# Kernel tuning notes

Measured on AMD Instinct MI355X. Metric: run time of the kernel, lower is better.

Reference implementation:

```python
import jax, jax.numpy as jnp
import numpy as np

N_NODES = 50000
N_EDGES = 800000
D_IN = 8
D_MODEL = 128
N_CLASSES = 2


def gcn_conv(x, W, b, src, dst, n_nodes):
    # PyG GCNConv: h = x @ W; add self-loops; D^{-1/2} A D^{-1/2} aggregation; + bias
    h = x @ W  # [N, D]
    deg = jax.ops.segment_sum(jnp.ones(src.shape[0], h.dtype), dst, num_segments=n_nodes) + 1.0  # +1 self-loop
    dinv = jax.lax.rsqrt(deg)  # deg >= 1 always
    norm = dinv[src] * dinv[dst]  # [E]
    agg = jax.ops.segment_sum(h[src] * norm[:, None], dst, num_segments=n_nodes)
    agg = agg + h * (dinv * dinv)[:, None]  # self-loop term, norm_ii = dinv_i^2
    return agg + b


def setup_inputs() -> dict:
    key = jax.random.key(0)
    ks = jax.random.split(key, 10)
    x = jax.random.normal(ks[0], (N_NODES, D_IN), jnp.float32)
    edge_index = jax.random.randint(ks[1], (2, N_EDGES), 0, N_NODES, jnp.int64 if jax.config.jax_enable_x64 else jnp.int32)
    def glorot(k, shape):
        lim = np.sqrt(6.0 / (shape[0] + shape[1]))
        return jax.random.uniform(k, shape, jnp.float32, -lim, lim)
    return {
        "x": x,
        "edge_index": edge_index,
        "W1": glorot(ks[2], (D_IN, D_MODEL)),
        "b1": jnp.zeros((D_MODEL,), jnp.float32),
        "W2": glorot(ks[3], (D_MODEL, D_MODEL)),
        "b2": jnp.zeros((D_MODEL,), jnp.float32),
        "Wlin1": glorot(ks[4], (2 * D_MODEL, D_MODEL)),
        "blin1": jnp.zeros((D_MODEL,), jnp.float32),
        "Wfin": glorot(ks[5], (D_MODEL, N_CLASSES)),
        "bfin": jnp.zeros((N_CLASSES,), jnp.float32),
    }


def reference(x, edge_index, W1, b1, W2, b2, Wlin1, blin1, Wfin, bfin):
    src, dst = edge_index[0], edge_index[1]
    n = x.shape[0]
    h = jax.nn.relu(gcn_conv(x, W1, b1, src, dst, n))
    h = jax.nn.relu(gcn_conv(h, W2, b2, src, dst, n))
    xpair = jnp.concatenate((h[src], h[dst]), axis=1)  # [E, 2*D]
    xpair = jax.nn.relu(xpair @ Wlin1 + blin1)
    logits = xpair @ Wfin + bfin  # [E, C]
    return jax.nn.log_softmax(logits, axis=1)
```

## Files before the change

kernel.cpp:

```cpp
#include <hip/hip_runtime.h>
#include <stdint.h>
#include <math.h>

#define D 128

typedef unsigned short u16;
typedef __attribute__((ext_vector_type(8))) short bf16x8;
typedef __attribute__((ext_vector_type(4))) float f32x4;
typedef __attribute__((ext_vector_type(2))) float f32x2;

union BU { uint4 u; bf16x8 s; };

__device__ __forceinline__ unsigned f2bf_pk(float a, float b) {
    union { float f; unsigned u; } x, y; x.f = a; y.f = b;
    unsigned ra = x.u + 0x7FFF + ((x.u >> 16) & 1);
    unsigned rb = y.u + 0x7FFF + ((y.u >> 16) & 1);
    return (ra >> 16) | (rb & 0xFFFF0000u);
}
__device__ __forceinline__ u16 f2bf(float f) {
    union { float f; unsigned u; } x; x.f = f;
    unsigned r = x.u + 0x7FFF + ((x.u >> 16) & 1);
    return (u16)(r >> 16);
}
__device__ __forceinline__ f32x2 bf2f2v(unsigned u) {
    union { unsigned w[2]; f32x2 v; } t;
    t.w[0] = u << 16; t.w[1] = u & 0xFFFF0000u;
    return t.v;
}
__device__ __forceinline__ f32x2 vmax0(f32x2 a) {
    return __builtin_elementwise_max(a, (f32x2)(0.f));
}
__device__ __forceinline__ int padded4(int deg) {
    return (deg + 3) & ~3;
}


__global__ __launch_bounds__(256) void k_degree8(const int* __restrict__ dst, int E,
                                                 int* __restrict__ hist8, u16* __restrict__ rank, int N,
                                                 int eb4,
                                                 const float* __restrict__ W2, const float* __restrict__ Wlin,
                                                 unsigned* __restrict__ wswz) {
    int b = blockIdx.x;
    int t = threadIdx.x;
    if (b < eb4) {
        int i = b * 256 + t;
        int copy = b & 7;
        int E4 = E >> 2;
        if (i < E4) {
            int4 d = ((const int4*)dst)[i];
            int* h = hist8 + copy * N;
            ushort4 rk;
            rk.x = (u16)atomicAdd(&h[d.x], 1);
            rk.y = (u16)atomicAdd(&h[d.y], 1);
            rk.z = (u16)atomicAdd(&h[d.z], 1);
            rk.w = (u16)atomicAdd(&h[d.w], 1);
            ((ushort4*)rank)[i] = rk;
        }
        if (i == 0) {
            for (int j = E4 * 4; j < E; ++j) rank[j] = (u16)atomicAdd(&hist8[dst[j]], 1);
        }
    } else {
        int tid = (b - eb4) * 256 + t;
        int m = tid >> 13;
        int r = tid & 8191;
        int jp = r & 3;
        int lane = (r >> 2) & 63;
        int ct = (r >> 8) & 7;
        int kc = r >> 11;
        int k0 = kc * 32 + (lane >> 4) * 8 + 2 * jp;
        int n = ct * 16 + (lane & 15);
        const float* srcp = (m == 0) ? W2 : (Wlin + (m - 1) * 16384);
        wswz[tid] = f2bf_pk(srcp[k0 * 128 + n], srcp[(k0 + 1) * 128 + n]);
    }
}

__global__ __launch_bounds__(256) void k_xcdoff_bsum(int* __restrict__ hist8, int* __restrict__ degi,
                                                     float* __restrict__ dinv, int* __restrict__ bsum, int N,
                                                     const float* __restrict__ x, float* __restrict__ xs) {
    __shared__ int ws[4];
    int t = threadIdx.x;
    int i = blockIdx.x * 256 + t;
    int pd = 0;
    if (i < N) {
        int run = 0;
#pragma unroll
        for (int j = 0; j < 8; ++j) {
            int c = hist8[j * N + i];
            hist8[j * N + i] = run;
            run += c;
        }
        degi[i] = run;
        float dv = rsqrtf((float)run + 1.0f);
        dinv[i] = dv;
        const float4* xp = (const float4*)(x + (size_t)i * 8);
        float4 a0 = xp[0], a1 = xp[1];
        float4 w0 = make_float4(dv * a0.x, dv * a0.y, dv * a0.z, dv * a0.w);
        float4 w1 = make_float4(dv * a1.x, dv * a1.y, dv * a1.z, dv * a1.w);
        float4* xo = (float4*)(xs + (size_t)i * 8);
        xo[0] = w0; xo[1] = w1;
        pd = padded4(run);
    } else if (i == N) {
        float4 z = make_float4(0.f, 0.f, 0.f, 0.f);
        float4* xo = (float4*)(xs + (size_t)N * 8);
        xo[0] = z; xo[1] = z;
    }
    int v = pd;
#pragma unroll
    for (int off = 1; off < 64; off <<= 1) v += __shfl_xor(v, off, 64);
    if ((t & 63) == 0) ws[t >> 6] = v;
    __syncthreads();
    if (t == 0) bsum[blockIdx.x] = ws[0] + ws[1] + ws[2] + ws[3];
}

__global__ __launch_bounds__(256) void k_scan_final(const int* __restrict__ degi, const int* __restrict__ bsum,
                                                    int* __restrict__ prow, int N, int* __restrict__ hist8,
                                                    int nb) {
    __shared__ int s[256];
    __shared__ int sb[256];
    int t = threadIdx.x;
    sb[t] = (t < nb) ? bsum[t] : 0;
    __syncthreads();
    for (int off = 1; off < 256; off <<= 1) {
        int v = (t >= off) ? sb[t - off] : 0;
        __syncthreads();
        sb[t] += v;
        __syncthreads();
    }
    int boff = (blockIdx.x == 0) ? 0 : sb[blockIdx.x - 1];

    int i = blockIdx.x * 256 + t;
    int pd = (i < N) ? padded4(degi[i]) : 0;
    s[t] = pd;
    __syncthreads();
    for (int off = 1; off < 256; off <<= 1) {
        int v = (t >= off) ? s[t - off] : 0;
        __syncthreads();
        s[t] += v;
        __syncthreads();
    }
    if (i < N) {
        int p = boff + ((t == 0) ? 0 : s[t - 1]);
        prow[i] = p;
#pragma unroll
        for (int j = 0; j < 8; ++j) hist8[j * N + i] += p;
    }
    if (blockIdx.x == (unsigned)(nb - 1) && t == 0) prow[N] = sb[nb - 1];
}


__global__ __launch_bounds__(256) void k_scatter_fill(
        const int* __restrict__ src, const int* __restrict__ dst, int E,
        const int* __restrict__ prow, const int* __restrict__ hist8, const u16* __restrict__ rank,
        const int* __restrict__ degi,
        u16* __restrict__ colsrc, int N, int eb4) {
    int t = threadIdx.x;
    int b = blockIdx.x;
    if (b < eb4) {
        int i = b * 256 + t;
        int E4 = E >> 2;
        if (i < E4) {
            int copy = b & 7;
            int4 d = ((const int4*)dst)[i];
            int4 s4 = ((const int4*)src)[i];
            ushort4 rk = ((const ushort4*)rank)[i];
            const int* h = hist8 + copy * N;
            colsrc[h[d.x] + rk.x] = (u16)s4.x;
            colsrc[h[d.y] + rk.y] = (u16)s4.y;
            colsrc[h[d.z] + rk.z] = (u16)s4.z;
            colsrc[h[d.w] + rk.w] = (u16)s4.w;
        }
        if (i == 0) {
            for (int j = E4 * 4; j < E; ++j)
                colsrc[hist8[dst[j]] + rank[j]] = (u16)src[j];
        }
    } else {
        int n = (b - eb4) * 256 + t;
        if (n < N) {
            int lo = prow[n];
            int deg = degi[n];
            int pd = padded4(deg);
            for (int j = deg; j < pd; ++j) colsrc[lo + j] = (u16)N;
        }
        if (b == eb4 && t == 0) {
            int P = prow[N];
            for (int j = 0; j < 16; ++j) colsrc[P + j] = (u16)N;
        }
    }
}

#define HROW 136


__global__ __launch_bounds__(256) void k_agg1gemm(
        const float* __restrict__ xs, const int* __restrict__ prow,
        const u16* __restrict__ colsrc, const float* __restrict__ dinv,
        const float* __restrict__ b1, const float* __restrict__ W1,
        const uint4* __restrict__ wB0, u16* __restrict__ out0, int N) {
    __shared__ float W1s[8 * 128];
    __shared__ float b1s[128];
    __shared__ float ys[16][8];
    __shared__ u16 hs[16 * HROW];
    int t = threadIdx.x;
    int wv = t >> 6;
    int lane = t & 63;
    int sub = lane >> 4;
    int r = lane & 15;
    int base = blockIdx.x * 16;

    for (int idx = t; idx < 8 * 128; idx += 256) W1s[idx] = W1[idx];
    if (t < 128) b1s[t] = b1[t];

    int i = base + wv * 4 + sub;
    if (i < N) {
        float acc[8];
#pragma unroll
        for (int f = 0; f < 8; ++f) acc[f] = 0.f;
        int lo = prow[i], hiP = prow[i + 1];
        for (int k = lo + r; k < hiP; k += 16) {
            int cj = colsrc[k];
            const float4* xr = (const float4*)(xs + (size_t)cj * 8);
            float4 u0 = xr[0], u1 = xr[1];
            acc[0] += u0.x; acc[1] += u0.y; acc[2] += u0.z; acc[3] += u0.w;
            acc[4] += u1.x; acc[5] += u1.y; acc[6] += u1.z; acc[7] += u1.w;
        }
#pragma unroll
        for (int off = 1; off < 16; off <<= 1) {
#pragma unroll
            for (int f = 0; f < 8; ++f) acc[f] += __shfl_xor(acc[f], off, 64);
        }
        const float4* xi = (const float4*)(xs + (size_t)i * 8);
        float4 s0 = xi[0], s1 = xi[1];
        float di = dinv[i];
        acc[0] = di * (acc[0] + s0.x); acc[1] = di * (acc[1] + s0.y);
        acc[2] = di * (acc[2] + s0.z); acc[3] = di * (acc[3] + s0.w);
        acc[4] = di * (acc[4] + s1.x); acc[5] = di * (acc[5] + s1.y);
        acc[6] = di * (acc[6] + s1.z); acc[7] = di * (acc[7] + s1.w);
        if (r < 8) ys[wv * 4 + sub][r] = acc[r];
    }
    __syncthreads();

    {
        int node16 = t >> 4;
        int cseg = (t & 15) * 8;
        if (base + node16 < N) {
            float yv[8];
#pragma unroll
            for (int f = 0; f < 8; ++f) yv[f] = ys[node16][f];
            float o[8];
#pragma unroll
            for (int c = 0; c < 8; ++c) {
                float s = b1s[cseg + c];
#pragma unroll
                for (int f = 0; f < 8; ++f) s += yv[f] * W1s[f * 128 + cseg + c];
                o[c] = fmaxf(s, 0.f);
            }
            uint4 ov;
            ov.x = f2bf_pk(o[0], o[1]);
            ov.y = f2bf_pk(o[2], o[3]);
            ov.z = f2bf_pk(o[4], o[5]);
            ov.w = f2bf_pk(o[6], o[7]);
            *(uint4*)(hs + node16 * HROW + cseg) = ov;
        } else {
            *(uint4*)(hs + node16 * HROW + cseg) = make_uint4(0, 0, 0, 0);
        }
    }
    __syncthreads();

    int quad = lane >> 4;
    int l15 = lane & 15;
    int ct0 = wv * 2;

    f32x4 accA[2];
#pragma unroll
    for (int q = 0; q < 2; ++q) accA[q] = (f32x4){0.f, 0.f, 0.f, 0.f};

    const uint4* hrow = (const uint4*)(hs + l15 * HROW);
#pragma unroll
    for (int kc = 0; kc < 4; ++kc) {
        BU a; a.u = hrow[kc * 4 + quad];
#pragma unroll
        for (int q = 0; q < 2; ++q) {
            BU b0; b0.u = wB0[(kc * 8 + ct0 + q) * 64 + lane];
            accA[q] = __builtin_amdgcn_mfma_f32_16x16x32_bf16(a.s, b0.s, accA[q], 0, 0, 0);
        }
    }
#pragma unroll
    for (int reg = 0; reg < 4; ++reg) {
        int node = base + quad * 4 + reg;
        if (node >= N) continue;
        float sc = dinv[node];
#pragma unroll
        for (int q = 0; q < 2; ++q) {
            int colj = (ct0 + q) * 16 + l15;
            out0[(size_t)node * 128 + colj] = f2bf(accA[q][reg] * sc);
        }
    }
    if (blockIdx.x == 0 && t < 64) ((unsigned*)out0)[(size_t)N * 64 + t] = 0;
}


template <bool DUAL>
__global__ __launch_bounds__(256) void k_aggemm(const uint4* __restrict__ g, const int* __restrict__ prow,
                                                const u16* __restrict__ colsrc, const float* __restrict__ dinv,
                                                const float* __restrict__ biasH,
                                                const uint4* __restrict__ wB0, const uint4* __restrict__ wB1,
                                                const float* __restrict__ bias1,
                                                u16* __restrict__ out0, u16* __restrict__ out1, int N) {
    __shared__ u16 hs[16 * HROW];
    int t = threadIdx.x;
    int wv = t >> 6;
    int lane = t & 63;
    int sub = lane >> 4;
    int r = lane & 15;
    int base = blockIdx.x * 16;

    for (int nd = 0; nd < 4; ++nd) {
        int i = base + wv * 4 + nd;
        int lrow = wv * 4 + nd;
        if (i < N) {
            f32x2 acc2[4];
#pragma unroll
            for (int j = 0; j < 4; ++j) acc2[j] = (f32x2)(0.f);
            int lo = prow[i], hiP = prow[i + 1];
            int idx = lo + sub;
            int c0 = colsrc[idx];
            int c1 = (idx + 4 < hiP) ? colsrc[idx + 4] : N;
            int c2 = (idx + 8 < hiP) ? colsrc[idx + 8] : N;
            uint4 v0 = g[c0 * 16 + r];
            uint4 v1 = g[c1 * 16 + r];
            for (int k = lo; k < hiP; k += 4) {
                int c3 = (idx + 12 < hiP) ? colsrc[idx + 12] : N;
                uint4 v2 = g[c2 * 16 + r];
                acc2[0] += bf2f2v(v0.x);
                acc2[1] += bf2f2v(v0.y);
                acc2[2] += bf2f2v(v0.z);
                acc2[3] += bf2f2v(v0.w);
                v0 = v1; v1 = v2; c2 = c3; idx += 4;
            }
#pragma unroll
            for (int j = 0; j < 4; ++j) {
                acc2[j].x += __shfl_xor(acc2[j].x, 16, 64);
                acc2[j].y += __shfl_xor(acc2[j].y, 16, 64);
                acc2[j].x += __shfl_xor(acc2[j].x, 32, 64);
                acc2[j].y += __shfl_xor(acc2[j].y, 32, 64);
            }
            if (sub == 0) {
                uint4 sv = g[i * 16 + r];
                acc2[0] += bf2f2v(sv.x);
                acc2[1] += bf2f2v(sv.y);
                acc2[2] += bf2f2v(sv.z);
                acc2[3] += bf2f2v(sv.w);
                float di = dinv[i];
                float4 b0 = ((const float4*)biasH)[r * 2];
                float4 b1v = ((const float4*)biasH)[r * 2 + 1];
                float r0 = fmaxf(acc2[0].x * di + b0.x, 0.f);
                float r1 = fmaxf(acc2[0].y * di + b0.y, 0.f);
                float r2 = fmaxf(acc2[1].x * di + b0.z, 0.f);
                float r3 = fmaxf(acc2[1].y * di + b0.w, 0.f);
                float r4 = fmaxf(acc2[2].x * di + b1v.x, 0.f);
                float r5 = fmaxf(acc2[2].y * di + b1v.y, 0.f);
                float r6 = fmaxf(acc2[3].x * di + b1v.z, 0.f);
                float r7 = fmaxf(acc2[3].y * di + b1v.w, 0.f);
                uint4 o;
                o.x = f2bf_pk(r0, r1);
                o.y = f2bf_pk(r2, r3);
                o.z = f2bf_pk(r4, r5);
                o.w = f2bf_pk(r6, r7);
                *(uint4*)(hs + lrow * HROW + r * 8) = o;
            }
        } else if (sub == 0) {
            *(uint4*)(hs + lrow * HROW + r * 8) = make_uint4(0, 0, 0, 0);
        }
    }
    __syncthreads();

    int quad = lane >> 4;
    int l15 = lane & 15;
    int ct0 = wv * 2;

    f32x4 accA[2], accB[2];
#pragma unroll
    for (int q = 0; q < 2; ++q) { accA[q] = (f32x4){0.f, 0.f, 0.f, 0.f}; accB[q] = (f32x4){0.f, 0.f, 0.f, 0.f}; }

    const uint4* hrow = (const uint4*)(hs + l15 * HROW);
#pragma unroll
    for (int kc = 0; kc < 4; ++kc) {
        BU a; a.u = hrow[kc * 4 + quad];
#pragma unroll
        for (int q = 0; q < 2; ++q) {
            BU b0; b0.u = wB0[(kc * 8 + ct0 + q) * 64 + lane];
            accA[q] = __builtin_amdgcn_mfma_f32_16x16x32_bf16(a.s, b0.s, accA[q], 0, 0, 0);
            if (DUAL) {
                BU b1; b1.u = wB1[(kc * 8 + ct0 + q) * 64 + lane];
                accB[q] = __builtin_amdgcn_mfma_f32_16x16x32_bf16(a.s, b1.s, accB[q], 0, 0, 0);
            }
        }
    }
#pragma unroll
    for (int reg = 0; reg < 4; ++reg) {
        int node = base + quad * 4 + reg;
        if (node >= N) continue;
        float sc = DUAL ? 1.0f : dinv[node];
#pragma unroll
        for (int q = 0; q < 2; ++q) {
            int colj = (ct0 + q) * 16 + l15;
            out0[(size_t)node * 128 + colj] = f2bf(accA[q][reg] * sc);
            if (DUAL) out1[(size_t)node * 128 + colj] = f2bf(accB[q][reg] + bias1[colj]);
        }
    }
    if (blockIdx.x == 0 && t < 64) ((unsigned*)out0)[(size_t)N * 64 + t] = 0;
}


__global__ __launch_bounds__(256) void k_edge(const uint4* __restrict__ a, const uint4* __restrict__ c,
                                              const int* __restrict__ src, const int* __restrict__ dst,
                                              const float* __restrict__ Wfin, const float* __restrict__ bfin,
                                              float* __restrict__ out, int E) {
    int t = threadIdx.x;
    int g = t >> 4;
    int r = t & 15;
    int base = blockIdx.x * 64 + g * 4;

    f32x2 wd[4];
    const float4* wvp = (const float4*)Wfin;
#pragma unroll
    for (int q = 0; q < 4; ++q) {
        float4 m = wvp[r * 4 + q];
        wd[q] = (f32x2){m.x - m.y, m.z - m.w};
    }
    float bd = bfin[0] - bfin[1];

    int4 s4, d4;
    if (base + 3 < E) {
        s4 = ((const int4*)src)[blockIdx.x * 16 + g];
        d4 = ((const int4*)dst)[blockIdx.x * 16 + g];
    } else {
        int e0 = base, e1 = base + 1, e2 = base + 2, e3 = base + 3;
        s4.x = (e0 < E) ? src[e0] : 0; d4.x = (e0 < E) ? dst[e0] : 0;
        s4.y = (e1 < E) ? src[e1] : 0; d4.y = (e1 < E) ? dst[e1] : 0;
        s4.z = (e2 < E) ? src[e2] : 0; d4.z = (e2 < E) ? dst[e2] : 0;
        s4.w = (e3 < E) ? src[e3] : 0; d4.w = (e3 < E) ? dst[e3] : 0;
    }

    uint4 av[4], cv[4];
    av[0] = a[(size_t)s4.x * 16 + r];  cv[0] = c[(size_t)d4.x * 16 + r];
    av[1] = a[(size_t)s4.y * 16 + r];  cv[1] = c[(size_t)d4.y * 16 + r];
    av[2] = a[(size_t)s4.z * 16 + r];  cv[2] = c[(size_t)d4.z * 16 + r];
    av[3] = a[(size_t)s4.w * 16 + r];  cv[3] = c[(size_t)d4.w * 16 + r];

    float dl[4];
#pragma unroll
    for (int j = 0; j < 4; ++j) {
        f32x2 p = (f32x2)(0.f);
        f32x2 z;
        z = vmax0(bf2f2v(av[j].x) + bf2f2v(cv[j].x)); p += z * wd[0];
        z = vmax0(bf2f2v(av[j].y) + bf2f2v(cv[j].y)); p += z * wd[1];
        z = vmax0(bf2f2v(av[j].z) + bf2f2v(cv[j].z)); p += z * wd[2];
        z = vmax0(bf2f2v(av[j].w) + bf2f2v(cv[j].w)); p += z * wd[3];
        dl[j] = p.x + p.y;
    }
#pragma unroll
    for (int off = 1; off < 16; off <<= 1) {
#pragma unroll
        for (int j = 0; j < 4; ++j) dl[j] += __shfl_xor(dl[j], off, 64);
    }
    if (r == 0) {
        float o[8];
#pragma unroll
        for (int j = 0; j < 4; ++j) {
            float dlt = dl[j] + bd;
            float tn = -fabsf(dlt);
            float s = __logf(1.f + __expf(tn));
            o[2 * j]     = (dlt >= 0.f) ? -s : (dlt - s);
            o[2 * j + 1] = (dlt >= 0.f) ? (-dlt - s) : -s;
        }
        if (base + 3 < E) {
            float4* op = (float4*)(out + 2 * (size_t)base);
            op[0] = make_float4(o[0], o[1], o[2], o[3]);
            op[1] = make_float4(o[4], o[5], o[6], o[7]);
        } else {
#pragma unroll
            for (int j = 0; j < 4; ++j) {
                if (base + j < E)
                    *((float2*)(out + 2 * (size_t)(base + j))) = make_float2(o[2 * j], o[2 * j + 1]);
            }
        }
    }
}

extern "C" void kernel_launch(void* const* d_in, const int* in_sizes, int n_in,
                              void* d_out, int out_size, void* d_ws, size_t ws_size,
                              hipStream_t stream) {
    const float* x     = (const float*)d_in[0];
    const int*   ei    = (const int*)d_in[1];
    const float* W1    = (const float*)d_in[2];
    const float* b1    = (const float*)d_in[3];
    const float* W2    = (const float*)d_in[4];
    const float* b2    = (const float*)d_in[5];
    const float* Wlin1 = (const float*)d_in[6];
    const float* blin1 = (const float*)d_in[7];
    const float* Wfin  = (const float*)d_in[8];
    const float* bfin  = (const float*)d_in[9];
    float* out = (float*)d_out;

    int N = in_sizes[0] / 8;
    int E = in_sizes[1] / 2;
    const int* src = ei;
    const int* dst = ei + E;
    int nb = (N + 255) / 256;
    int eb4 = (E / 4 + 255) / 256;

#define ALIGN256(p) (char*)(((uintptr_t)(p) + 255) & ~(uintptr_t)255)
    char* w = (char*)d_ws;
    int* hist8 = (int*)w;     w += (size_t)8 * N * 4;
    u16* rank = (u16*)w;      w += (size_t)E * 2;
    w = ALIGN256(w);
    int* degi = (int*)w;      w += (size_t)N * 4;
    int* prow = (int*)w;      w += (size_t)(N + 1) * 4;
    float* dinv = (float*)w;  w += (size_t)N * 4;
    int* bsum = (int*)w;      w += (size_t)nb * 4;
    w = ALIGN256(w);
    u16* colsrc = (u16*)w;    w += ((size_t)E + 8 * (size_t)N + 64) * 2;
    w = ALIGN256(w);
    unsigned* wswz = (unsigned*)w; w += (size_t)3 * 8192 * 4;
    w = ALIGN256(w);
    float* xs = (float*)w;    w += (size_t)(N + 1) * 8 * 4;
    w = ALIGN256(w);
    unsigned* bufA = (unsigned*)w; w += (size_t)(N + 1) * 64 * 4;
    w = ALIGN256(w);
    unsigned* bufC = (unsigned*)w; w += (size_t)N * 64 * 4;
    w = ALIGN256(w);
    unsigned* bufG2 = (unsigned*)w; w += (size_t)(N + 1) * 64 * 4;

    hipMemsetAsync(hist8, 0, (size_t)8 * N * 4, stream);

    k_degree8<<<eb4 + 96, 256, 0, stream>>>(dst, E, hist8, rank, N, eb4, W2, Wlin1, wswz);
    k_xcdoff_bsum<<<nb, 256, 0, stream>>>(hist8, degi, dinv, bsum, N, x, xs);
    k_scan_final<<<nb, 256, 0, stream>>>(degi, bsum, prow, N, hist8, nb);
    k_scatter_fill<<<eb4 + nb, 256, 0, stream>>>(src, dst, E, prow, hist8, rank, degi,
                                                 colsrc, N, eb4);

    int ablocks = (N + 15) / 16;
    k_agg1gemm<<<ablocks, 256, 0, stream>>>(xs, prow, colsrc, dinv, b1, W1,
                                            (const uint4*)wswz, (u16*)bufG2, N);
    k_aggemm<true><<<ablocks, 256, 0, stream>>>((const uint4*)bufG2, prow, colsrc, dinv, b2,
                                                (const uint4*)(wswz + 8192), (const uint4*)(wswz + 16384),
                                                blin1, (u16*)bufA, (u16*)bufC, N);

    k_edge<<<(E + 63) / 64, 256, 0, stream>>>((const uint4*)bufA, (const uint4*)bufC,
                                              src, dst, Wfin, bfin, out, E);
}
```

Before: 246.8 us.

## Replace 8-copy degree histogram and two-pass scan with single-pass decoupled lookback scan

Drops the eight per-XCD histogram copies in favour of one shared count array with atomics. It also merges the block-sum and final-scan kernels into one kernel that chains block prefixes through a look-back array of flagged 64-bit entries, and moves the padding fill into that kernel. This removes one kernel launch and the extra passes over the 8×N histogram. In exchange, atomics on a single copy see more contention, and the look-back spin-wait assumes earlier blocks are scheduled first.

Result: slower. 253.5 us (+2.8%).

```diff
diff --git a/kernel.cpp b/kernel.cpp
--- a/kernel.cpp
+++ b/kernel.cpp
@@ -5,6 +5,7 @@
 #define D 128
 
 typedef unsigned short u16;
+typedef unsigned long long u64;
 typedef __attribute__((ext_vector_type(8))) short bf16x8;
 typedef __attribute__((ext_vector_type(4))) float f32x4;
 typedef __attribute__((ext_vector_type(2))) float f32x2;
@@ -35,29 +36,27 @@
 }
 
 
-__global__ __launch_bounds__(256) void k_degree8(const int* __restrict__ dst, int E,
-                                                 int* __restrict__ hist8, u16* __restrict__ rank, int N,
-                                                 int eb4,
-                                                 const float* __restrict__ W2, const float* __restrict__ Wlin,
-                                                 unsigned* __restrict__ wswz) {
+__global__ __launch_bounds__(256) void k_degree(const int* __restrict__ dst, int E,
+                                                int* __restrict__ cnt, u16* __restrict__ rank,
+                                                int eb4,
+                                                const float* __restrict__ W2, const float* __restrict__ Wlin,
+                                                unsigned* __restrict__ wswz) {
     int b = blockIdx.x;
     int t = threadIdx.x;
     if (b < eb4) {
         int i = b * 256 + t;
-        int copy = b & 7;
         int E4 = E >> 2;
         if (i < E4) {
             int4 d = ((const int4*)dst)[i];
-            int* h = hist8 + copy * N;
             ushort4 rk;
-            rk.x = (u16)atomicAdd(&h[d.x], 1);
-            rk.y = (u16)atomicAdd(&h[d.y], 1);
-            rk.z = (u16)atomicAdd(&h[d.z], 1);
-            rk.w = (u16)atomicAdd(&h[d.w], 1);
+            rk.x = (u16)atomicAdd(&cnt[d.x], 1);
+            rk.y = (u16)atomicAdd(&cnt[d.y], 1);
+            rk.z = (u16)atomicAdd(&cnt[d.z], 1);
+            rk.w = (u16)atomicAdd(&cnt[d.w], 1);
             ((ushort4*)rank)[i] = rk;
         }
-        if (i == 0) {
-            for (int j = E4 * 4; j < E; ++j) rank[j] = (u16)atomicAdd(&hist8[dst[j]], 1);
+        if (b == 0 && t == 0) {
+            for (int j = E4 * 4; j < E; ++j) rank[j] = (u16)atomicAdd(&cnt[dst[j]], 1);
         }
     } else {
         int tid = (b - eb4) * 256 + t;
@@ -74,22 +73,19 @@
     }
 }
 
-__global__ __launch_bounds__(256) void k_xcdoff_bsum(int* __restrict__ hist8, int* __restrict__ degi,
-                                                     float* __restrict__ dinv, int* __restrict__ bsum, int N,
-                                                     const float* __restrict__ x, float* __restrict__ xs) {
-    __shared__ int ws[4];
+
+__global__ __launch_bounds__(256) void k_scanall(
+        const int* __restrict__ cnt, float* __restrict__ dinv, int* __restrict__ prow,
+        int N, int nb, const float* __restrict__ x, float* __restrict__ xs,
+        u16* __restrict__ colsrc, u64* __restrict__ look) {
+    __shared__ int s[256];
+    __shared__ int basesh;
     int t = threadIdx.x;
-    int i = blockIdx.x * 256 + t;
-    int pd = 0;
+    int b = blockIdx.x;
+    int i = b * 256 + t;
+    int run = 0, pd = 0;
     if (i < N) {
-        int run = 0;
-#pragma unroll
-        for (int j = 0; j < 8; ++j) {
-            int c = hist8[j * N + i];
-            hist8[j * N + i] = run;
-            run += c;
-        }
-        degi[i] = run;
+        run = cnt[i];
         float dv = rsqrtf((float)run + 1.0f);
         dinv[i] = dv;
         const float4* xp = (const float4*)(x + (size_t)i * 8);
@@ -104,32 +100,6 @@
         float4* xo = (float4*)(xs + (size_t)N * 8);
         xo[0] = z; xo[1] = z;
     }
-    int v = pd;
-#pragma unroll
-    for (int off = 1; off < 64; off <<= 1) v += __shfl_xor(v, off, 64);
-    if ((t & 63) == 0) ws[t >> 6] = v;
-    __syncthreads();
-    if (t == 0) bsum[blockIdx.x] = ws[0] + ws[1] + ws[2] + ws[3];
-}
-
-__global__ __launch_bounds__(256) void k_scan_final(const int* __restrict__ degi, const int* __restrict__ bsum,
-                                                    int* __restrict__ prow, int N, int* __restrict__ hist8,
-                                                    int nb) {
-    __shared__ int s[256];
-    __shared__ int sb[256];
-    int t = threadIdx.x;
-    sb[t] = (t < nb) ? bsum[t] : 0;
-    __syncthreads();
-    for (int off = 1; off < 256; off <<= 1) {
-        int v = (t >= off) ? sb[t - off] : 0;
-        __syncthreads();
-        sb[t] += v;
-        __syncthreads();
-    }
-    int boff = (blockIdx.x == 0) ? 0 : sb[blockIdx.x - 1];
-
-    int i = blockIdx.x * 256 + t;
-    int pd = (i < N) ? padded4(degi[i]) : 0;
     s[t] = pd;
     __syncthreads();
     for (int off = 1; off < 256; off <<= 1) {
@@ -138,53 +108,56 @@
         s[t] += v;
         __syncthreads();
     }
+    int Ssum = s[255];
+    if (t == 0)
+        __hip_atomic_store(&look[b], (1ull << 32) | (u64)(unsigned)Ssum,
+                           __ATOMIC_RELEASE, __HIP_MEMORY_SCOPE_AGENT);
+    if (t < 64) {
+        int acc = 0;
+        for (int j = b - 1 - t; j >= 0; j -= 64) {
+            u64 v;
+            do {
+                v = __hip_atomic_load(&look[j], __ATOMIC_ACQUIRE, __HIP_MEMORY_SCOPE_AGENT);
+            } while (!(v >> 32));
+            acc += (int)(unsigned)v;
+        }
+#pragma unroll
+        for (int off = 1; off < 64; off <<= 1) acc += __shfl_xor(acc, off, 64);
+        if (t == 0) basesh = acc;
+    }
+    __syncthreads();
+    int base = basesh;
     if (i < N) {
-        int p = boff + ((t == 0) ? 0 : s[t - 1]);
+        int p = base + ((t == 0) ? 0 : s[t - 1]);
         prow[i] = p;
-#pragma unroll
-        for (int j = 0; j < 8; ++j) hist8[j * N + i] += p;
-    }
-    if (blockIdx.x == (unsigned)(nb - 1) && t == 0) prow[N] = sb[nb - 1];
-}
-
-
-__global__ __launch_bounds__(256) void k_scatter_fill(
+        for (int j = run; j < pd; ++j) colsrc[p + j] = (u16)N;
+    }
+    if (b == nb - 1 && t == 0) {
+        int P = base + Ssum;
+        prow[N] = P;
+        for (int j = 0; j < 16; ++j) colsrc[P + j] = (u16)N;
+    }
+}
+
+
+__global__ __launch_bounds__(256) void k_scatter(
         const int* __restrict__ src, const int* __restrict__ dst, int E,
-        const int* __restrict__ prow, const int* __restrict__ hist8, const u16* __restrict__ rank,
-        const int* __restrict__ degi,
-        u16* __restrict__ colsrc, int N, int eb4) {
-    int t = threadIdx.x;
-    int b = blockIdx.x;
-    if (b < eb4) {
-        int i = b * 256 + t;
-        int E4 = E >> 2;
-        if (i < E4) {
-            int copy = b & 7;
-            int4 d = ((const int4*)dst)[i];
-            int4 s4 = ((const int4*)src)[i];
-            ushort4 rk = ((const ushort4*)rank)[i];
-            const int* h = hist8 + copy * N;
-            colsrc[h[d.x] + rk.x] = (u16)s4.x;
-            colsrc[h[d.y] + rk.y] = (u16)s4.y;
-            colsrc[h[d.z] + rk.z] = (u16)s4.z;
-            colsrc[h[d.w] + rk.w] = (u16)s4.w;
-        }
-        if (i == 0) {
-            for (int j = E4 * 4; j < E; ++j)
-                colsrc[hist8[dst[j]] + rank[j]] = (u16)src[j];
-        }
-    } else {
-        int n = (b - eb4) * 256 + t;
-        if (n < N) {
-            int lo = prow[n];
-            int deg = degi[n];
-            int pd = padded4(deg);
-            for (int j = deg; j < pd; ++j) colsrc[lo + j] = (u16)N;
-        }
-        if (b == eb4 && t == 0) {
-            int P = prow[N];
-            for (int j = 0; j < 16; ++j) colsrc[P + j] = (u16)N;
-        }
+        const int* __restrict__ prow, const u16* __restrict__ rank,
+        u16* __restrict__ colsrc) {
+    int i = blockIdx.x * 256 + threadIdx.x;
+    int E4 = E >> 2;
+    if (i < E4) {
+        int4 d = ((const int4*)dst)[i];
+        int4 s4 = ((const int4*)src)[i];
+        ushort4 rk = ((const ushort4*)rank)[i];
+        colsrc[prow[d.x] + rk.x] = (u16)s4.x;
+        colsrc[prow[d.y] + rk.y] = (u16)s4.y;
+        colsrc[prow[d.z] + rk.z] = (u16)s4.z;
+        colsrc[prow[d.w] + rk.w] = (u16)s4.w;
+    }
+    if (i == 0) {
+        for (int j = E4 * 4; j < E; ++j)
+            colsrc[prow[dst[j]] + rank[j]] = (u16)src[j];
     }
 }
 
@@ -512,13 +485,12 @@
 
 #define ALIGN256(p) (char*)(((uintptr_t)(p) + 255) & ~(uintptr_t)255)
     char* w = (char*)d_ws;
-    int* hist8 = (int*)w;     w += (size_t)8 * N * 4;
+    int* cnt = (int*)w;       w += (size_t)N * 4;
+    u64* look = (u64*)w;      w += (size_t)nb * 8;
     u16* rank = (u16*)w;      w += (size_t)E * 2;
     w = ALIGN256(w);
-    int* degi = (int*)w;      w += (size_t)N * 4;
     int* prow = (int*)w;      w += (size_t)(N + 1) * 4;
     float* dinv = (float*)w;  w += (size_t)N * 4;
-    int* bsum = (int*)w;      w += (size_t)nb * 4;
     w = ALIGN256(w);
     u16* colsrc = (u16*)w;    w += ((size_t)E + 8 * (size_t)N + 64) * 2;
     w = ALIGN256(w);
@@ -532,13 +504,11 @@
     w = ALIGN256(w);
     unsigned* bufG2 = (unsigned*)w; w += (size_t)(N + 1) * 64 * 4;
 
-    hipMemsetAsync(hist8, 0, (size_t)8 * N * 4, stream);
-
-    k_degree8<<<eb4 + 96, 256, 0, stream>>>(dst, E, hist8, rank, N, eb4, W2, Wlin1, wswz);
-    k_xcdoff_bsum<<<nb, 256, 0, stream>>>(hist8, degi, dinv, bsum, N, x, xs);
-    k_scan_final<<<nb, 256, 0, stream>>>(degi, bsum, prow, N, hist8, nb);
-    k_scatter_fill<<<eb4 + nb, 256, 0, stream>>>(src, dst, E, prow, hist8, rank, degi,
-                                                 colsrc, N, eb4);
+    hipMemsetAsync(cnt, 0, (size_t)N * 4 + (size_t)nb * 8, stream);
+
+    k_degree<<<eb4 + 96, 256, 0, stream>>>(dst, E, cnt, rank, eb4, W2, Wlin1, wswz);
+    k_scanall<<<nb, 256, 0, stream>>>(cnt, dinv, prow, N, nb, x, xs, colsrc, look);
+    k_scatter<<<eb4, 256, 0, stream>>>(src, dst, E, prow, rank, colsrc);
 
     int ablocks = (N + 15) / 16;
     k_agg1gemm<<<ablocks, 256, 0, stream>>>(xs, prow, colsrc, dinv, b1, W1,
```
